# Performance work log

Hardware: AMD Instinct MI355X
Metric: run time of the kernel (lower is better)

## Reference

```python
import jax, jax.numpy as jnp
import numpy as np

N = 50000        # nodes
E = 800000       # edges (before self loops)
G = 512          # graphs
H = 2            # heads
FIN = 128        # in_features
CH = 64          # hidden per head
COUT = 32        # out_features
NEG_SLOPE = 0.2  # PyG GATConv default
BN_EPS = 1e-5


def _gat(x, src, dst, W, a_src, a_dst, b, concat, n):
    # x: [n, F], W: [F, H*C], a_src/a_dst: [H, C]
    h = (x @ W).reshape(n, a_src.shape[0], a_src.shape[1])        # [n, H, C]
    e = jax.nn.leaky_relu((h * a_src).sum(-1)[src]
                          + (h * a_dst).sum(-1)[dst], NEG_SLOPE)  # [Etot, H]
    # per-destination segment softmax (self loops guarantee nonempty segments)
    m = jax.ops.segment_max(e, dst, num_segments=n)
    ex = jnp.exp(e - m[dst])
    s = jax.ops.segment_sum(ex, dst, num_segments=n)
    alpha = ex / (s[dst] + 1e-16)                                 # [Etot, H]
    out = jax.ops.segment_sum(h[src] * alpha[:, :, None], dst, num_segments=n)
    out = out.reshape(n, -1) if concat else out.mean(axis=1)
    return out + b


def _bn(x, gamma, beta, mean, var):
    # BatchNorm1d in eval mode (running statistics)
    return (x - mean) * jax.lax.rsqrt(var + BN_EPS) * gamma + beta


def setup_inputs() -> dict:
    key = jax.random.key(0)
    ks = jax.random.split(key, 12)
    x = jax.random.normal(ks[0], (N, FIN), dtype=jnp.float32)
    edge_index = jax.random.randint(ks[1], (2, E), 0, N, dtype=jnp.int32)
    batch = jnp.sort(jax.random.randint(ks[2], (N,), 0, G, dtype=jnp.int32))
    inp = {"x": x, "edge_index": edge_index, "batch": batch}
    # layer 1: GATConv(FIN -> CH, heads=H, concat=True)
    inp["W1"] = jax.random.normal(ks[3], (FIN, H * CH), dtype=jnp.float32) * 0.1
    inp["as1"] = jax.random.normal(ks[4], (H, CH), dtype=jnp.float32) * 0.1
    inp["ad1"] = jax.random.normal(ks[5], (H, CH), dtype=jnp.float32) * 0.1
    inp["b1"] = jnp.zeros((H * CH,), dtype=jnp.float32)
    inp["bn1_gamma"] = jnp.ones((H * CH,), dtype=jnp.float32)
    inp["bn1_beta"] = jnp.zeros((H * CH,), dtype=jnp.float32)
    inp["bn1_mean"] = jax.random.normal(ks[6], (H * CH,), dtype=jnp.float32) * 0.05
    inp["bn1_var"] = jnp.ones((H * CH,), dtype=jnp.float32)
    # layer 2: GATConv(H*CH -> COUT, heads=H, concat=False)
    inp["W2"] = jax.random.normal(ks[7], (H * CH, H * COUT), dtype=jnp.float32) * 0.1
    inp["as2"] = jax.random.normal(ks[8], (H, COUT), dtype=jnp.float32) * 0.1
    inp["ad2"] = jax.random.normal(ks[9], (H, COUT), dtype=jnp.float32) * 0.1
    inp["b2"] = jnp.zeros((COUT,), dtype=jnp.float32)
    inp["bn2_gamma"] = jnp.ones((COUT,), dtype=jnp.float32)
    inp["bn2_beta"] = jnp.zeros((COUT,), dtype=jnp.float32)
    inp["bn2_mean"] = jax.random.normal(ks[10], (COUT,), dtype=jnp.float32) * 0.05
    inp["bn2_var"] = jnp.ones((COUT,), dtype=jnp.float32)
    return inp


def reference(x, edge_index, batch,
              W1, as1, ad1, b1, bn1_gamma, bn1_beta, bn1_mean, bn1_var,
              W2, as2, ad2, b2, bn2_gamma, bn2_beta, bn2_mean, bn2_var):
    n = x.shape[0]
    sl = jnp.arange(n, dtype=edge_index.dtype)
    src = jnp.concatenate([edge_index[0], sl])  # PyG add_self_loops=True
    dst = jnp.concatenate([edge_index[1], sl])
    h = _gat(x, src, dst, W1, as1, ad1, b1, True, n)
    h = jax.nn.relu(_bn(h, bn1_gamma, bn1_beta, bn1_mean, bn1_var))
    h = _gat(h, src, dst, W2, as2, ad2, b2, False, n)
    h = _bn(h, bn2_gamma, bn2_beta, bn2_mean, bn2_var)
    # global mean pool over graphs
    sums = jax.ops.segment_sum(h, batch, num_segments=G)
    cnts = jax.ops.segment_sum(jnp.ones((n,), h.dtype), batch, num_segments=G)
    pooled = sums / jnp.maximum(cnts, 1.0)[:, None]
    return jax.nn.log_softmax(pooled, axis=1)
```

## Files before the change

kernel.cpp:

```cpp
#include <hip/hip_runtime.h>
#include <hip/hip_bf16.h>

#define NEG_SLOPE 0.2f
#define BN_EPS 1e-5f
#define BSHIFT 7
#define P_PART 256
#define MAXB 512

typedef unsigned int uint32;
typedef unsigned short ushort16;
typedef __attribute__((ext_vector_type(8))) short bf16x8;
typedef __attribute__((ext_vector_type(4))) float f32x4;

__device__ __forceinline__ ushort16 f2bf(float f) {
    uint32 u = __float_as_uint(f);
    u = (u + 0x7fff + ((u >> 16) & 1)) >> 16;
    return (ushort16)u;
}
__device__ __forceinline__ float bfu_lo(uint32 u) { return __uint_as_float(u << 16); }
__device__ __forceinline__ float bfu_hi(uint32 u) { return __uint_as_float(u & 0xffff0000u); }

__global__ __launch_bounds__(256) void hist_part(const int* __restrict__ ei, int E, int Etot,
                                                 int nbuck, int chunk, int* __restrict__ hist) {
    const int p = blockIdx.x;
    __shared__ int lh[MAXB];
    for (int i = threadIdx.x; i < nbuck; i += 256) lh[i] = 0;
    __syncthreads();
    const int beg = p * chunk;
    const int end = min(beg + chunk, Etot);
    for (int i = beg + threadIdx.x; i < end; i += 256) {
        int d = (i < E) ? ei[E + i] : i - E;
        atomicAdd(&lh[d >> BSHIFT], 1);
    }
    __syncthreads();
    for (int i = threadIdx.x; i < nbuck; i += 256) hist[(size_t)i * P_PART + p] = lh[i];
}

__global__ __launch_bounds__(P_PART) void row_scan(int* __restrict__ hist,
                                                   int* __restrict__ rowtot) {
    const int b = blockIdx.x;
    __shared__ int s[P_PART];
    const int t = threadIdx.x;
    int v = hist[(size_t)b * P_PART + t];
    s[t] = v;
    __syncthreads();
    for (int off = 1; off < P_PART; off <<= 1) {
        int u = (t >= off) ? s[t - off] : 0;
        __syncthreads();
        s[t] += u;
        __syncthreads();
    }
    hist[(size_t)b * P_PART + t] = s[t] - v;
    if (t == P_PART - 1) rowtot[b] = s[t];
}

__global__ __launch_bounds__(512) void tot_scan(const int* __restrict__ rowtot,
                                                int* __restrict__ bbase, int nbuck, int Etot) {
    __shared__ int s[512];
    const int t = threadIdx.x;
    int v = (t < nbuck) ? rowtot[t] : 0;
    s[t] = v;
    __syncthreads();
    for (int off = 1; off < 512; off <<= 1) {
        int u = (t >= off) ? s[t - off] : 0;
        __syncthreads();
        s[t] += u;
        __syncthreads();
    }
    if (t < nbuck) bbase[t] = s[t] - v;
    if (t == 0) bbase[nbuck] = Etot;
}

__global__ __launch_bounds__(256) void rank_scatter(const int* __restrict__ ei, int E, int Etot,
                                                    int nbuck, int chunk,
                                                    const int* __restrict__ hist,
                                                    const int* __restrict__ bbase,
                                                    uint32* __restrict__ ebuf) {
    const int p = blockIdx.x;
    __shared__ int cur[MAXB];
    for (int i = threadIdx.x; i < nbuck; i += 256)
        cur[i] = bbase[i] + hist[(size_t)i * P_PART + p];
    __syncthreads();
    const int beg = p * chunk;
    const int end = min(beg + chunk, Etot);
    for (int i = beg + threadIdx.x; i < end; i += 256) {
        int s_, d_;
        if (i < E) { s_ = ei[i]; d_ = ei[E + i]; }
        else       { s_ = d_ = i - E; }
        int pos = atomicAdd(&cur[d_ >> BSHIFT], 1);
        ebuf[pos] = ((uint32)(d_ & ((1 << BSHIFT) - 1)) << 25) | (uint32)s_;
    }
}

__global__ __launch_bounds__(256) void bucket_place(
    const int* __restrict__ bbase, const uint32* __restrict__ ebuf, int N,
    int* __restrict__ base, int* __restrict__ csr_src) {
    const int bk = blockIdx.x;
    __shared__ int ldeg[1 << BSHIFT];
    __shared__ int sscan[1 << BSHIFT];
    __shared__ int lcur[1 << BSHIFT];
    const int t = threadIdx.x;
    if (t < (1 << BSHIFT)) { ldeg[t] = 0; lcur[t] = 0; }
    __syncthreads();
    const int beg = bbase[bk], end = bbase[bk + 1];
    for (int i = beg + t; i < end; i += 256) atomicAdd(&ldeg[ebuf[i] >> 25], 1);
    __syncthreads();
    if (t < 128) sscan[t] = ldeg[t];
    __syncthreads();
    for (int off = 1; off < 128; off <<= 1) {
        int v = 0;
        if (t < 128 && t >= off) v = sscan[t - off];
        __syncthreads();
        if (t < 128) sscan[t] += v;
        __syncthreads();
    }
    if (t < 128) {
        int node = (bk << BSHIFT) + t;
        if (node < N) base[node] = beg + sscan[t] - ldeg[t];
    }
    __syncthreads();
    for (int i = beg + t; i < end; i += 256) {
        uint32 pk = ebuf[i];
        int dl = (int)(pk >> 25);
        int s_ = (int)(pk & 0x1FFFFFFu);
        int pos = beg + (sscan[dl] - ldeg[dl]) + atomicAdd(&lcur[dl], 1);
        csr_src[pos] = s_;
    }
}

__global__ void graph_bounds(const int* __restrict__ batch, int N, int G,
                             int* __restrict__ gstart) {
    int g = blockIdx.x * blockDim.x + threadIdx.x;
    if (g > G) return;
    if (g == G) { gstart[G] = N; return; }
    int lo = 0, hi = N;
    while (lo < hi) { int mid = (lo + hi) >> 1; if (batch[mid] < g) lo = mid + 1; else hi = mid; }
    gstart[g] = lo;
}

template <int OC, int C>
__global__ void pack_w(const float* __restrict__ W, const float* __restrict__ a_s,
                       const float* __restrict__ a_d, ushort16* __restrict__ wt) {
    const int col = blockIdx.x;
    const int k = threadIdx.x;
    float v = 0.f;
    if (col < OC) {
        v = W[k * OC + col];
    } else if (col < OC + 2) {
        int hh = col - OC;
        float s = 0.f;
        for (int c = 0; c < C; ++c) s += W[k * OC + hh * C + c] * a_s[hh * C + c];
        v = s;
    } else if (col < OC + 4) {
        int hh = col - OC - 2;
        float s = 0.f;
        for (int c = 0; c < C; ++c) s += W[k * OC + hh * C + c] * a_d[hh * C + c];
        v = s;
    }
    wt[(size_t)col * 128 + k] = f2bf(v);
}

template <int OC, int NT, bool AF32>
__global__ __launch_bounds__(256) void gemm_mfma(
    const void* __restrict__ xin, const ushort16* __restrict__ wt,
    ushort16* __restrict__ h, float4* __restrict__ att, float2* __restrict__ asc, int N) {
    const int wave = threadIdx.x >> 6, lane = threadIdx.x & 63;
    const int tile = blockIdx.x * 4 + wave;
    if (tile * 16 >= N) return;
    const int m = lane & 15, quad = lane >> 4;
    const int node = tile * 16 + m;

    bf16x8 a[4];
    if (AF32) {
        const float* xr = (const float*)xin + (size_t)node * 128 + quad * 8;
#pragma unroll
        for (int c = 0; c < 4; ++c) {
            float4 u = *(const float4*)(xr + c * 32);
            float4 v = *(const float4*)(xr + c * 32 + 4);
            bf16x8 t;
            t[0] = (short)f2bf(u.x); t[1] = (short)f2bf(u.y);
            t[2] = (short)f2bf(u.z); t[3] = (short)f2bf(u.w);
            t[4] = (short)f2bf(v.x); t[5] = (short)f2bf(v.y);
            t[6] = (short)f2bf(v.z); t[7] = (short)f2bf(v.w);
            a[c] = t;
        }
    } else {
        const ushort16* xr = (const ushort16*)xin + (size_t)node * 128 + quad * 8;
#pragma unroll
        for (int c = 0; c < 4; ++c) a[c] = *(const bf16x8*)(xr + c * 32);
    }

    for (int t = 0; t < NT; ++t) {
        const ushort16* wr = wt + ((size_t)(t * 16 + m)) * 128 + quad * 8;
        bf16x8 b[4];
#pragma unroll
        for (int c = 0; c < 4; ++c) b[c] = *(const bf16x8*)(wr + c * 32);
        f32x4 acc = {0.f, 0.f, 0.f, 0.f};
#pragma unroll
        for (int c = 0; c < 4; ++c)
            acc = __builtin_amdgcn_mfma_f32_16x16x32_bf16(a[c], b[c], acc, 0, 0, 0);
        if (t * 16 < OC) {
#pragma unroll
            for (int r = 0; r < 4; ++r) {
                int nrow = tile * 16 + quad * 4 + r;
                h[(size_t)nrow * OC + t * 16 + m] = f2bf(acc[r]);
            }
        } else if (m < 4) {
#pragma unroll
            for (int r = 0; r < 4; ++r) {
                int nrow = tile * 16 + quad * 4 + r;
                ((float*)(att + nrow))[m] = acc[r];
                if (m < 2) ((float*)(asc + nrow))[m] = acc[r];
            }
        }
    }
}

__global__ __launch_bounds__(256) void gat_gather1(
    const int* __restrict__ base, const int* __restrict__ csr_src, int Etot, int N,
    const ushort16* __restrict__ h, const float4* __restrict__ att,
    const float2* __restrict__ asc,
    const float* __restrict__ b, const float* __restrict__ g, const float* __restrict__ be,
    const float* __restrict__ mu, const float* __restrict__ var,
    ushort16* __restrict__ outb) {
    const int node = __builtin_amdgcn_readfirstlane(blockIdx.x * 4 + (threadIdx.x >> 6));
    if (node >= N) return;
    const int t = threadIdx.x & 63;
    const int sub = t >> 4;
    const int q = t & 15;
    const int hh = q >> 3;
    const int beg = base[node];
    const int end = (node + 1 < N) ? base[node + 1] : Etot;
    const int deg = end - beg;
    const int nk = (deg - sub + 3) >> 2;
    const int nkmax = (deg + 3) >> 2;
    const float4 adn = att[node];
    const float advh = hh ? adn.w : adn.z;

    float a0 = 0.f, a1 = 0.f, a2 = 0.f, a3 = 0.f;
    float a4 = 0.f, a5 = 0.f, a6 = 0.f, a7 = 0.f, ssum = 0.f;
    constexpr int U = 4;
    for (int k = 0; k < nkmax; k += U) {
        int sidx[U];
        float msk[U];
#pragma unroll
        for (int j = 0; j < U; ++j) {
            int kk = k + j;
            bool ok = kk < nk;
            sidx[j] = csr_src[beg + (ok ? 4 * kk + sub : 0)];
            msk[j] = ok ? 1.f : 0.f;
        }
        float2 av[U];
        uint4 hv[U];
#pragma unroll
        for (int j = 0; j < U; ++j) {
            av[j] = asc[sidx[j]];
            hv[j] = *(const uint4*)(h + (size_t)sidx[j] * 128 + 8 * q);
        }
#pragma unroll
        for (int j = 0; j < U; ++j) {
            float ev = (hh ? av[j].y : av[j].x) + advh;
            ev = ev > 0.f ? ev : NEG_SLOPE * ev;
            float ex = __expf(ev) * msk[j];
            a0 += ex * bfu_lo(hv[j].x);
            a1 += ex * bfu_hi(hv[j].x);
            a2 += ex * bfu_lo(hv[j].y);
            a3 += ex * bfu_hi(hv[j].y);
            a4 += ex * bfu_lo(hv[j].z);
            a5 += ex * bfu_hi(hv[j].z);
            a6 += ex * bfu_lo(hv[j].w);
            a7 += ex * bfu_hi(hv[j].w);
            ssum += ex;
        }
    }
#pragma unroll
    for (int off = 16; off <= 32; off <<= 1) {
        a0 += __shfl_xor(a0, off, 64);
        a1 += __shfl_xor(a1, off, 64);
        a2 += __shfl_xor(a2, off, 64);
        a3 += __shfl_xor(a3, off, 64);
        a4 += __shfl_xor(a4, off, 64);
        a5 += __shfl_xor(a5, off, 64);
        a6 += __shfl_xor(a6, off, 64);
        a7 += __shfl_xor(a7, off, 64);
        ssum += __shfl_xor(ssum, off, 64);
    }
    if (t < 16) {
        const float inv = 1.f / (ssum + 1e-16f);
        const int c0 = 8 * q;
        float va[8] = {a0, a1, a2, a3, a4, a5, a6, a7};
        uint32 pk[4];
#pragma unroll
        for (int i = 0; i < 8; i += 2) {
            float v0 = va[i] * inv + b[c0 + i];
            float v1 = va[i + 1] * inv + b[c0 + i + 1];
            v0 = fmaxf((v0 - mu[c0 + i]) * rsqrtf(var[c0 + i] + BN_EPS) * g[c0 + i] + be[c0 + i], 0.f);
            v1 = fmaxf((v1 - mu[c0 + i + 1]) * rsqrtf(var[c0 + i + 1] + BN_EPS) * g[c0 + i + 1] + be[c0 + i + 1], 0.f);
            pk[i >> 1] = (uint32)f2bf(v0) | ((uint32)f2bf(v1) << 16);
        }
        uint4 r = make_uint4(pk[0], pk[1], pk[2], pk[3]);
        *(uint4*)(outb + (size_t)node * 128 + c0) = r;
    }
}

__global__ __launch_bounds__(256) void gat_gather2(
    const int* __restrict__ base, const int* __restrict__ csr_src, int Etot, int N,
    const ushort16* __restrict__ h2, const float4* __restrict__ att,
    const float2* __restrict__ asc,
    const float* __restrict__ b2, const float* __restrict__ g, const float* __restrict__ be,
    const float* __restrict__ mu, const float* __restrict__ var,
    float* __restrict__ node_out) {
    const int node = __builtin_amdgcn_readfirstlane(blockIdx.x * 4 + (threadIdx.x >> 6));
    if (node >= N) return;
    const int t = threadIdx.x & 63;
    const int sub = t >> 4;
    const int q = t & 15;
    const int hh = q >> 3;
    const int beg = base[node];
    const int end = (node + 1 < N) ? base[node + 1] : Etot;
    const int deg = end - beg;
    const int nk = (deg - sub + 3) >> 2;
    const int nkmax = (deg + 3) >> 2;
    const float4 adn = att[node];
    const float advh = hh ? adn.w : adn.z;

    float a0 = 0.f, a1 = 0.f, a2 = 0.f, a3 = 0.f, ssum = 0.f;
    constexpr int U = 4;
    for (int k = 0; k < nkmax; k += U) {
        int sidx[U];
        float msk[U];
#pragma unroll
        for (int j = 0; j < U; ++j) {
            int kk = k + j;
            bool ok = kk < nk;
            sidx[j] = csr_src[beg + (ok ? 4 * kk + sub : 0)];
            msk[j] = ok ? 1.f : 0.f;
        }
        float2 av[U];
        uint2 hv[U];
#pragma unroll
        for (int j = 0; j < U; ++j) {
            av[j] = asc[sidx[j]];
            hv[j] = *(const uint2*)(h2 + (size_t)sidx[j] * 64 + 4 * q);
        }
#pragma unroll
        for (int j = 0; j < U; ++j) {
            float ev = (hh ? av[j].y : av[j].x) + advh;
            ev = ev > 0.f ? ev : NEG_SLOPE * ev;
            float ex = __expf(ev) * msk[j];
            a0 += ex * bfu_lo(hv[j].x);
            a1 += ex * bfu_hi(hv[j].x);
            a2 += ex * bfu_lo(hv[j].y);
            a3 += ex * bfu_hi(hv[j].y);
            ssum += ex;
        }
    }
#pragma unroll
    for (int off = 16; off <= 32; off <<= 1) {
        a0 += __shfl_xor(a0, off, 64);
        a1 += __shfl_xor(a1, off, 64);
        a2 += __shfl_xor(a2, off, 64);
        a3 += __shfl_xor(a3, off, 64);
        ssum += __shfl_xor(ssum, off, 64);
    }
    const float inv = 1.f / (ssum + 1e-16f);
    float v0 = a0 * inv, v1 = a1 * inv, v2 = a2 * inv, v3 = a3 * inv;
    const int src = (t & 15) + 8;
    float p0 = __shfl(v0, src, 64);
    float p1 = __shfl(v1, src, 64);
    float p2 = __shfl(v2, src, 64);
    float p3 = __shfl(v3, src, 64);
    if (t < 8) {
        const int c0 = 4 * t;
        float m0 = 0.5f * (v0 + p0) + b2[c0];
        float m1 = 0.5f * (v1 + p1) + b2[c0 + 1];
        float m2 = 0.5f * (v2 + p2) + b2[c0 + 2];
        float m3 = 0.5f * (v3 + p3) + b2[c0 + 3];
        m0 = (m0 - mu[c0]) * rsqrtf(var[c0] + BN_EPS) * g[c0] + be[c0];
        m1 = (m1 - mu[c0 + 1]) * rsqrtf(var[c0 + 1] + BN_EPS) * g[c0 + 1] + be[c0 + 1];
        m2 = (m2 - mu[c0 + 2]) * rsqrtf(var[c0 + 2] + BN_EPS) * g[c0 + 2] + be[c0 + 2];
        m3 = (m3 - mu[c0 + 3]) * rsqrtf(var[c0 + 3] + BN_EPS) * g[c0 + 3] + be[c0 + 3];
        *(float4*)(node_out + (size_t)node * 32 + c0) = make_float4(m0, m1, m2, m3);
    }
}

__global__ __launch_bounds__(256) void pool_logsoftmax(
    const float* __restrict__ node_out, const int* __restrict__ gstart,
    float* __restrict__ out) {
    const int gidx = blockIdx.x;
    const int tid = threadIdx.x;
    const int c = tid & 31, r = tid >> 5;
    const int n0 = gstart[gidx], n1 = gstart[gidx + 1];
    float s = 0.f;
    for (int n = n0 + r; n < n1; n += 8) s += node_out[(size_t)n * 32 + c];
    __shared__ float red[8][32];
    red[r][c] = s;
    __syncthreads();
    if (r == 0) {
        float tot = red[0][c];
#pragma unroll
        for (int k = 1; k < 8; ++k) tot += red[k][c];
        float v = tot / fmaxf((float)(n1 - n0), 1.f);
        float m = v;
#pragma unroll
        for (int off = 16; off >= 1; off >>= 1) m = fmaxf(m, __shfl_xor(m, off, 64));
        float ex = __expf(v - m);
        float ssum = ex;
#pragma unroll
        for (int off = 16; off >= 1; off >>= 1) ssum += __shfl_xor(ssum, off, 64);
        out[gidx * 32 + c] = v - m - logf(ssum);
    }
}

extern "C" void kernel_launch(void* const* d_in, const int* in_sizes, int n_in,
                              void* d_out, int out_size, void* d_ws, size_t ws_size,
                              hipStream_t stream) {
    const float* x   = (const float*)d_in[0];
    const int* ei    = (const int*)d_in[1];
    const int* batch = (const int*)d_in[2];
    const float* W1  = (const float*)d_in[3];
    const float* as1 = (const float*)d_in[4];
    const float* ad1 = (const float*)d_in[5];
    const float* b1  = (const float*)d_in[6];
    const float* g1  = (const float*)d_in[7];
    const float* be1 = (const float*)d_in[8];
    const float* mu1 = (const float*)d_in[9];
    const float* vr1 = (const float*)d_in[10];
    const float* W2  = (const float*)d_in[11];
    const float* as2 = (const float*)d_in[12];
    const float* ad2 = (const float*)d_in[13];
    const float* b2  = (const float*)d_in[14];
    const float* g2  = (const float*)d_in[15];
    const float* be2 = (const float*)d_in[16];
    const float* mu2 = (const float*)d_in[17];
    const float* vr2 = (const float*)d_in[18];
    float* out = (float*)d_out;

    const int N = in_sizes[0] / 128;
    const int E = in_sizes[1] / 2;
    const int Etot = E + N;
    const int G = out_size / 32;
    const int nbuck = (N + (1 << BSHIFT) - 1) >> BSHIFT;
    const int chunk = (Etot + P_PART - 1) / P_PART;
    const int M = nbuck * P_PART;
    const int ntile = (N + 15) / 16;
    const int gemm_grid = (ntile + 3) / 4;

    float* p = (float*)d_ws;
    size_t o = 0;
    auto al = [&]() { o = (o + 3) & ~(size_t)3; };
    ushort16* h1b   = (ushort16*)(p + o); o += (size_t)N * 64;  al();
    ushort16* agg1b = (ushort16*)(p + o); o += (size_t)N * 64;  al();
    ushort16* h2b   = (ushort16*)(p + o); o += (size_t)N * 32;  al();
    float4* att1 = (float4*)(p + o); o += (size_t)N * 4;  al();
    float4* att2 = (float4*)(p + o); o += (size_t)N * 4;  al();
    float2* asc1 = (float2*)(p + o); o += (size_t)N * 2;  al();
    float2* asc2 = (float2*)(p + o); o += (size_t)N * 2;  al();
    float* nodeo = p + o; o += (size_t)N * 32; al();
    ushort16* wt1 = (ushort16*)(p + o); o += (size_t)144 * 64; al();
    ushort16* wt2 = (ushort16*)(p + o); o += (size_t)80 * 64;  al();
    int* csr_src = (int*)(p + o); o += (size_t)Etot; al();
    uint32* ebuf = (uint32*)(p + o); o += (size_t)Etot; al();
    int* base    = (int*)(p + o); o += (size_t)N;    al();
    int* hist    = (int*)(p + o); o += (size_t)M;    al();
    int* rowtot  = (int*)(p + o); o += (size_t)nbuck + 4; al();
    int* bbase   = (int*)(p + o); o += (size_t)nbuck + 4; al();
    int* gstart  = (int*)(p + o); o += (size_t)G + 4; al();

    hist_part<<<P_PART, 256, 0, stream>>>(ei, E, Etot, nbuck, chunk, hist);
    row_scan<<<nbuck, P_PART, 0, stream>>>(hist, rowtot);
    tot_scan<<<1, 512, 0, stream>>>(rowtot, bbase, nbuck, Etot);
    rank_scatter<<<P_PART, 256, 0, stream>>>(ei, E, Etot, nbuck, chunk, hist, bbase, ebuf);
    bucket_place<<<nbuck, 256, 0, stream>>>(bbase, ebuf, N, base, csr_src);
    graph_bounds<<<(G + 256) / 256, 256, 0, stream>>>(batch, N, G, gstart);
    pack_w<128, 64><<<144, 128, 0, stream>>>(W1, as1, ad1, wt1);
    pack_w<64, 32><<<80, 128, 0, stream>>>(W2, as2, ad2, wt2);

    gemm_mfma<128, 9, true><<<gemm_grid, 256, 0, stream>>>(x, wt1, h1b, att1, asc1, N);
    gat_gather1<<<(N + 3) / 4, 256, 0, stream>>>(base, csr_src, Etot, N, h1b, att1, asc1,
                                                 b1, g1, be1, mu1, vr1, agg1b);
    gemm_mfma<64, 5, false><<<gemm_grid, 256, 0, stream>>>(agg1b, wt2, h2b, att2, asc2, N);
    gat_gather2<<<(N + 3) / 4, 256, 0, stream>>>(base, csr_src, Etot, N, h2b, att2, asc2,
                                                 b2, g2, be2, mu2, vr2, nodeo);

    pool_logsoftmax<<<G, 256, 0, stream>>>(nodeo, gstart, out);
}
```

Before: 257.7 us.

## Compute edge attention weights once per lane and broadcast via shuffles in GAT gathers

Both gather kernels now load up to 64 edge source indices at once with one lane per edge. Each lane computes both heads' exp-weights, and the softmax denominators come from a wave-wide butterfly reduction. The feature-gather loop then takes the source index and weight for each edge by shuffle instead of reloading csr_src and asc and recomputing exp 16 times per edge. This removes redundant scattered loads and transcendental work, but adds many shuffle instructions and an extra full-wave reduction per 64-edge chunk.

```diff
diff --git a/kernel.cpp b/kernel.cpp
--- a/kernel.cpp
+++ b/kernel.cpp
@@ -232,45 +232,57 @@
     const int beg = base[node];
     const int end = (node + 1 < N) ? base[node + 1] : Etot;
     const int deg = end - beg;
-    const int nk = (deg - sub + 3) >> 2;
-    const int nkmax = (deg + 3) >> 2;
     const float4 adn = att[node];
-    const float advh = hh ? adn.w : adn.z;
 
     float a0 = 0.f, a1 = 0.f, a2 = 0.f, a3 = 0.f;
-    float a4 = 0.f, a5 = 0.f, a6 = 0.f, a7 = 0.f, ssum = 0.f;
-    constexpr int U = 4;
-    for (int k = 0; k < nkmax; k += U) {
-        int sidx[U];
-        float msk[U];
-#pragma unroll
-        for (int j = 0; j < U; ++j) {
-            int kk = k + j;
-            bool ok = kk < nk;
-            sidx[j] = csr_src[beg + (ok ? 4 * kk + sub : 0)];
-            msk[j] = ok ? 1.f : 0.f;
-        }
-        float2 av[U];
-        uint4 hv[U];
-#pragma unroll
-        for (int j = 0; j < U; ++j) {
-            av[j] = asc[sidx[j]];
-            hv[j] = *(const uint4*)(h + (size_t)sidx[j] * 128 + 8 * q);
-        }
-#pragma unroll
-        for (int j = 0; j < U; ++j) {
-            float ev = (hh ? av[j].y : av[j].x) + advh;
-            ev = ev > 0.f ? ev : NEG_SLOPE * ev;
-            float ex = __expf(ev) * msk[j];
-            a0 += ex * bfu_lo(hv[j].x);
-            a1 += ex * bfu_hi(hv[j].x);
-            a2 += ex * bfu_lo(hv[j].y);
-            a3 += ex * bfu_hi(hv[j].y);
-            a4 += ex * bfu_lo(hv[j].z);
-            a5 += ex * bfu_hi(hv[j].z);
-            a6 += ex * bfu_lo(hv[j].w);
-            a7 += ex * bfu_hi(hv[j].w);
-            ssum += ex;
+    float a4 = 0.f, a5 = 0.f, a6 = 0.f, a7 = 0.f;
+    float ssum0 = 0.f, ssum1 = 0.f;
+
+    for (int c0e = 0; c0e < deg; c0e += 64) {
+        const int rel = c0e + t;
+        const bool ok = rel < deg;
+        const int sidxme = csr_src[beg + (ok ? rel : 0)];
+        const float2 av = asc[sidxme];
+        float e0 = av.x + adn.z, e1 = av.y + adn.w;
+        e0 = e0 > 0.f ? e0 : NEG_SLOPE * e0;
+        e1 = e1 > 0.f ? e1 : NEG_SLOPE * e1;
+        const float x0 = ok ? __expf(e0) : 0.f;
+        const float x1 = ok ? __expf(e1) : 0.f;
+        float r0 = x0, r1 = x1;
+#pragma unroll
+        for (int off = 1; off < 64; off <<= 1) {
+            r0 += __shfl_xor(r0, off, 64);
+            r1 += __shfl_xor(r1, off, 64);
+        }
+        ssum0 += r0;
+        ssum1 += r1;
+        const int degc = min(deg - c0e, 64);
+        const int kkmax = (degc + 3) >> 2;
+        for (int kk = 0; kk < kkmax; kk += 4) {
+            int sidx[4];
+            float exv[4];
+            uint4 hv[4];
+#pragma unroll
+            for (int j = 0; j < 4; ++j) {
+                int sl = min(4 * (kk + j) + sub, 63);
+                sidx[j] = __shfl(sidxme, sl, 64);
+                float f0 = __shfl(x0, sl, 64);
+                float f1 = __shfl(x1, sl, 64);
+                exv[j] = hh ? f1 : f0;
+                hv[j] = *(const uint4*)(h + (size_t)sidx[j] * 128 + 8 * q);
+            }
+#pragma unroll
+            for (int j = 0; j < 4; ++j) {
+                const float ex = exv[j];
+                a0 += ex * bfu_lo(hv[j].x);
+                a1 += ex * bfu_hi(hv[j].x);
+                a2 += ex * bfu_lo(hv[j].y);
+                a3 += ex * bfu_hi(hv[j].y);
+                a4 += ex * bfu_lo(hv[j].z);
+                a5 += ex * bfu_hi(hv[j].z);
+                a6 += ex * bfu_lo(hv[j].w);
+                a7 += ex * bfu_hi(hv[j].w);
+            }
         }
     }
 #pragma unroll
@@ -283,10 +295,9 @@
         a5 += __shfl_xor(a5, off, 64);
         a6 += __shfl_xor(a6, off, 64);
         a7 += __shfl_xor(a7, off, 64);
-        ssum += __shfl_xor(ssum, off, 64);
     }
     if (t < 16) {
-        const float inv = 1.f / (ssum + 1e-16f);
+        const float inv = 1.f / ((hh ? ssum1 : ssum0) + 1e-16f);
         const int c0 = 8 * q;
         float va[8] = {a0, a1, a2, a3, a4, a5, a6, a7};
         uint32 pk[4];
@@ -319,40 +330,52 @@
     const int beg = base[node];
     const int end = (node + 1 < N) ? base[node + 1] : Etot;
     const int deg = end - beg;
-    const int nk = (deg - sub + 3) >> 2;
-    const int nkmax = (deg + 3) >> 2;
     const float4 adn = att[node];
-    const float advh = hh ? adn.w : adn.z;
-
-    float a0 = 0.f, a1 = 0.f, a2 = 0.f, a3 = 0.f, ssum = 0.f;
-    constexpr int U = 4;
-    for (int k = 0; k < nkmax; k += U) {
-        int sidx[U];
-        float msk[U];
-#pragma unroll
-        for (int j = 0; j < U; ++j) {
-            int kk = k + j;
-            bool ok = kk < nk;
-            sidx[j] = csr_src[beg + (ok ? 4 * kk + sub : 0)];
-            msk[j] = ok ? 1.f : 0.f;
-        }
-        float2 av[U];
-        uint2 hv[U];
-#pragma unroll
-        for (int j = 0; j < U; ++j) {
-            av[j] = asc[sidx[j]];
-            hv[j] = *(const uint2*)(h2 + (size_t)sidx[j] * 64 + 4 * q);
-        }
-#pragma unroll
-        for (int j = 0; j < U; ++j) {
-            float ev = (hh ? av[j].y : av[j].x) + advh;
-            ev = ev > 0.f ? ev : NEG_SLOPE * ev;
-            float ex = __expf(ev) * msk[j];
-            a0 += ex * bfu_lo(hv[j].x);
-            a1 += ex * bfu_hi(hv[j].x);
-            a2 += ex * bfu_lo(hv[j].y);
-            a3 += ex * bfu_hi(hv[j].y);
-            ssum += ex;
+
+    float a0 = 0.f, a1 = 0.f, a2 = 0.f, a3 = 0.f;
+    float ssum0 = 0.f, ssum1 = 0.f;
+
+    for (int c0e = 0; c0e < deg; c0e += 64) {
+        const int rel = c0e + t;
+        const bool ok = rel < deg;
+        const int sidxme = csr_src[beg + (ok ? rel : 0)];
+        const float2 av = asc[sidxme];
+        float e0 = av.x + adn.z, e1 = av.y + adn.w;
+        e0 = e0 > 0.f ? e0 : NEG_SLOPE * e0;
+        e1 = e1 > 0.f ? e1 : NEG_SLOPE * e1;
+        const float x0 = ok ? __expf(e0) : 0.f;
+        const float x1 = ok ? __expf(e1) : 0.f;
+        float r0 = x0, r1 = x1;
+#pragma unroll
+        for (int off = 1; off < 64; off <<= 1) {
+            r0 += __shfl_xor(r0, off, 64);
+            r1 += __shfl_xor(r1, off, 64);
+        }
+        ssum0 += r0;
+        ssum1 += r1;
+        const int degc = min(deg - c0e, 64);
+        const int kkmax = (degc + 3) >> 2;
+        for (int kk = 0; kk < kkmax; kk += 4) {
+            int sidx[4];
+            float exv[4];
+            uint2 hv[4];
+#pragma unroll
+            for (int j = 0; j < 4; ++j) {
+                int sl = min(4 * (kk + j) + sub, 63);
+                sidx[j] = __shfl(sidxme, sl, 64);
+                float f0 = __shfl(x0, sl, 64);
+                float f1 = __shfl(x1, sl, 64);
+                exv[j] = hh ? f1 : f0;
+                hv[j] = *(const uint2*)(h2 + (size_t)sidx[j] * 64 + 4 * q);
+            }
+#pragma unroll
+            for (int j = 0; j < 4; ++j) {
+                const float ex = exv[j];
+                a0 += ex * bfu_lo(hv[j].x);
+                a1 += ex * bfu_hi(hv[j].x);
+                a2 += ex * bfu_lo(hv[j].y);
+                a3 += ex * bfu_hi(hv[j].y);
+            }
         }
     }
 #pragma unroll
@@ -361,9 +384,8 @@
         a1 += __shfl_xor(a1, off, 64);
         a2 += __shfl_xor(a2, off, 64);
         a3 += __shfl_xor(a3, off, 64);
-        ssum += __shfl_xor(ssum, off, 64);
-    }
-    const float inv = 1.f / (ssum + 1e-16f);
+    }
+    const float inv = 1.f / ((hh ? ssum1 : ssum0) + 1e-16f);
     float v0 = a0 * inv, v1 = a1 * inv, v2 = a2 * inv, v3 = a3 * inv;
     const int src = (t & 15) + 8;
     float p0 = __shfl(v0, src, 64);
```

Result: faster. 250.0 us (-3.0%).
